# Kernel optimization log

Hardware: AMD Instinct MI355X
Metric: run time of the kernel (lower is better)

## Reference

```python
import jax, jax.numpy as jnp
import numpy as np

HID = 64
L = 5
N_NODES = 50000
N_EDGES = 1600000
N_GRAPHS = 4
EPS = 1e-5


def _ln(h, g, b):
    m = jnp.mean(h, axis=-1, keepdims=True)
    v = jnp.mean((h - m) ** 2, axis=-1, keepdims=True)
    return (h - m) * jax.lax.rsqrt(v + EPS) * g + b


def _lin_init(key, fan_in, fan_out):
    return jax.random.normal(key, (fan_in, fan_out), jnp.float32) / np.sqrt(fan_in)


def setup_inputs() -> dict:
    key = jax.random.key(0)
    ks = jax.random.split(key, 24)
    inp = {}
    inp['x'] = jax.random.normal(ks[0], (N_NODES, 8), jnp.float32)
    inp['edge_index'] = jax.random.randint(ks[1], (2, N_EDGES), 0, N_NODES)
    inp['edge_attr'] = jax.random.normal(ks[2], (N_EDGES, 5), jnp.float32)
    inp['batch'] = jnp.sort(jax.random.randint(ks[3], (N_NODES,), 0, N_GRAPHS))
    inp['case_params'] = jax.random.normal(ks[4], (N_GRAPHS, 4), jnp.float32)
    inp['bc_params'] = jax.random.normal(ks[5], (N_GRAPHS, 4), jnp.float32)
    # encoder
    inp['enc_W1'] = _lin_init(ks[6], 16, HID); inp['enc_b1'] = jnp.zeros((HID,))
    inp['enc_W2'] = _lin_init(ks[7], HID, HID); inp['enc_b2'] = jnp.zeros((HID,))
    inp['enc_g'] = jnp.ones((HID,)); inp['enc_be'] = jnp.zeros((HID,))
    # processor (stacked over L layers)
    ek = jax.random.split(ks[8], L); nk = jax.random.split(ks[9], L)
    ek2 = jax.random.split(ks[10], L); nk2 = jax.random.split(ks[11], L)
    inp['eW1'] = jnp.stack([_lin_init(ek[i], 2 * HID + 5, HID) for i in range(L)])
    inp['eb1'] = jnp.zeros((L, HID))
    inp['eW2'] = jnp.stack([_lin_init(ek2[i], HID, HID) for i in range(L)])
    inp['eb2'] = jnp.zeros((L, HID))
    inp['eg'] = jnp.ones((L, HID)); inp['ebe'] = jnp.zeros((L, HID))
    inp['nW1'] = jnp.stack([_lin_init(nk[i], 2 * HID, HID) for i in range(L)])
    inp['nb1'] = jnp.zeros((L, HID))
    inp['nW2'] = jnp.stack([_lin_init(nk2[i], HID, HID) for i in range(L)])
    inp['nb2'] = jnp.zeros((L, HID))
    inp['ng'] = jnp.ones((L, HID)); inp['nbe'] = jnp.zeros((L, HID))
    # decoders
    inp['dlW1'] = _lin_init(ks[12], HID, HID); inp['dlb1'] = jnp.zeros((HID,))
    inp['dlW2'] = _lin_init(ks[13], HID, 6); inp['dlb2'] = jnp.zeros((6,))
    inp['dgW1'] = _lin_init(ks[14], HID, HID // 2); inp['dgb1'] = jnp.zeros((HID // 2,))
    inp['dgW2'] = _lin_init(ks[15], HID // 2, 4); inp['dgb2'] = jnp.zeros((4,))
    return inp


def reference(x, edge_index, edge_attr, batch, case_params, bc_params,
              enc_W1, enc_b1, enc_W2, enc_b2, enc_g, enc_be,
              eW1, eb1, eW2, eb2, eg, ebe,
              nW1, nb1, nW2, nb2, ng, nbe,
              dlW1, dlb1, dlW2, dlb2, dgW1, dgb1, dgW2, dgb2):
    n_nodes = x.shape[0]
    n_graphs = case_params.shape[0]
    silu = jax.nn.silu
    # input concat: node feats + per-graph globals gathered by batch index
    gv = jnp.concatenate([case_params, bc_params], axis=1)  # [B, 8]
    h = jnp.concatenate([x, gv[batch]], axis=1)             # [N, 16]
    # encoder
    h = _ln(silu(h @ enc_W1 + enc_b1) @ enc_W2 + enc_b2, enc_g, enc_be)
    src, dst = edge_index[0], edge_index[1]  # PyG: x_j = src, x_i = dst
    n_layers = eW1.shape[0]
    for l in range(n_layers):
        xi = h[dst]  # [E, H] target
        xj = h[src]  # [E, H] source
        m = jnp.concatenate([xi, xj, edge_attr], axis=1)  # [E, 2H+5]
        m = _ln(silu(m @ eW1[l] + eb1[l]) @ eW2[l] + eb2[l], eg[l], ebe[l])
        agg = jax.ops.segment_sum(m, dst, num_segments=n_nodes)  # scatter-add
        t = jnp.concatenate([h, agg], axis=1)  # [N, 2H]
        h = h + _ln(silu(t @ nW1[l] + nb1[l]) @ nW2[l] + nb2[l], ng[l], nbe[l])
    out_local = silu(h @ dlW1 + dlb1) @ dlW2 + dlb2  # [N, 6]
    cnt = jax.ops.segment_sum(jnp.ones((n_nodes,), h.dtype), batch, num_segments=n_graphs)
    pooled = jax.ops.segment_sum(h, batch, num_segments=n_graphs) / jnp.maximum(cnt, 1.0)[:, None]
    out_global = silu(pooled @ dgW1 + dgb1) @ dgW2 + dgb2  # [B, 4]
    return (out_local, out_global)
```

## Files before the change

### kernel.cpp

```cpp
#include <hip/hip_runtime.h>
#include <cmath>

constexpr int NN = 50000;
constexpr int NE = 1600000;
constexpr int H  = 64;
constexpr int NL = 5;
constexpr int NG = 4;
constexpr int EIN = 2 * H + 5;
constexpr int NIN = 2 * H;

typedef short bf16x8 __attribute__((ext_vector_type(8)));
typedef float f32x4  __attribute__((ext_vector_type(4)));

__device__ __forceinline__ float silu_f(float x) {
    return x / (1.0f + __expf(-x));
}

__device__ __forceinline__ unsigned int f2bf(float f) {
    unsigned int u = __float_as_uint(f);
    u += 0x7fffu + ((u >> 16) & 1u);
    return u >> 16;
}
__device__ __forceinline__ unsigned int pack_bf16x2(float x, float y) {
    unsigned int r;
    asm("v_cvt_pk_bf16_f32 %0, %1, %2" : "=v"(r) : "v"(x), "v"(y));
    return r;
}

template <int CTRL>
__device__ __forceinline__ int dpp_i(int old, int v) {
    return __builtin_amdgcn_update_dpp(old, v, CTRL, 0xF, 0xF, false);
}

__global__ __launch_bounds__(256) void degree_kernel(
    const int* __restrict__ ei, int* __restrict__ deg)
{
    int e = blockIdx.x * 256 + threadIdx.x;
    if (e < NE) atomicAdd(&deg[ei[NE + e]], 1);
}

__global__ __launch_bounds__(1024) void scan1_kernel(
    const int* __restrict__ deg, int* __restrict__ off, int* __restrict__ bsum)
{
    __shared__ int sh[1024];
    const int tid = threadIdx.x;
    int i = blockIdx.x * 1024 + tid;
    int v = (i < NN) ? deg[i] : 0;
    sh[tid] = v;
    __syncthreads();
    for (int d = 1; d < 1024; d <<= 1) {
        int t = (tid >= d) ? sh[tid - d] : 0;
        __syncthreads();
        sh[tid] += t;
        __syncthreads();
    }
    if (i < NN) off[i] = sh[tid] - v;
    if (tid == 1023) bsum[blockIdx.x] = sh[1023];
}

__global__ __launch_bounds__(64) void scan2_kernel(
    const int* __restrict__ bsum, int* __restrict__ bbase, int nb)
{
    int lane = threadIdx.x;
    int v = (lane < nb) ? bsum[lane] : 0;
    int orig = v;
    for (int d = 1; d < 64; d <<= 1) {
        int t = __shfl_up(v, d);
        if (lane >= d) v += t;
    }
    bbase[lane] = v - orig;
}

__global__ __launch_bounds__(1024) void scan3_kernel(
    int* __restrict__ off, const int* __restrict__ bbase,
    int* __restrict__ cursor)
{
    int i = blockIdx.x * 1024 + threadIdx.x;
    if (i < NN) {
        int o = off[i] + bbase[blockIdx.x];
        off[i] = o;
        cursor[i] = o;
        if (i == NN - 1) off[NN] = NE;
    }
}

__global__ __launch_bounds__(256) void scatter_kernel(
    const int* __restrict__ ei, int* __restrict__ cursor,
    int* __restrict__ sidx, int* __restrict__ sdst, int* __restrict__ ssrc)
{
    int e = blockIdx.x * 256 + threadIdx.x;
    if (e < NE) {
        int d = ei[NE + e];
        int p = atomicAdd(&cursor[d], 1);
        sidx[p] = e;
        sdst[p] = d;
        ssrc[p] = ei[e];
    }
}

__global__ __launch_bounds__(256) void ea_pack_kernel(
    const float* __restrict__ ea, const int* __restrict__ sidx,
    uint4* __restrict__ ea_pk)
{
    int p = blockIdx.x * 256 + threadIdx.x;
    if (p < NE) {
        const float* s = ea + (size_t)sidx[p] * 5;
        uint4 v;
        v.x = pack_bf16x2(s[0], s[1]);
        v.y = pack_bf16x2(s[2], s[3]);
        v.z = pack_bf16x2(s[4], 0.0f);
        v.w = 0u;
        ea_pk[p] = v;
    }
}

__global__ __launch_bounds__(256) void pack_weights_kernel(
    const float* __restrict__ eW1, const float* __restrict__ eW2,
    const float* __restrict__ nW1, const float* __restrict__ nW2,
    const float* __restrict__ dlW1, const float* __restrict__ dlW2,
    short* __restrict__ eW1pk, short* __restrict__ eW2pk,
    short* __restrict__ nW1pk, short* __restrict__ nW2pk,
    short* __restrict__ dlW1pk, short* __restrict__ dlW2pk)
{
    int l = blockIdx.y;
    int t = blockIdx.x * 256 + threadIdx.x;
    if (t < 10240) {
        int j = t & 7, lane = (t >> 3) & 63, mt = (t >> 9) & 3, ks = t >> 11;
        int k  = ks * 32 + (lane >> 4) * 8 + j;
        int ch = mt * 16 + (lane & 15);
        float v = (k < EIN) ? eW1[(size_t)l * EIN * H + k * H + ch] : 0.0f;
        eW1pk[(size_t)l * 10240 + t] = (short)f2bf(v);
    } else if (t < 14336) {
        int t2 = t - 10240;
        int j = t2 & 7, lane = (t2 >> 3) & 63, mt = (t2 >> 9) & 3, ks = t2 >> 11;
        int k = ks * 32 + (lane >> 4) * 8 + j;
        int ch = mt * 16 + (lane & 15);
        eW2pk[(size_t)l * 4096 + t2] = (short)f2bf(eW2[(size_t)l * H * H + k * H + ch]);
    } else if (t < 22528) {
        int t3 = t - 14336;
        int j = t3 & 7, lane = (t3 >> 3) & 63, mt = (t3 >> 9) & 3, ks = t3 >> 11;
        int k = ks * 32 + (lane >> 4) * 8 + j;
        int ch = mt * 16 + (lane & 15);
        nW1pk[(size_t)l * 8192 + t3] = (short)f2bf(nW1[(size_t)l * NIN * H + k * H + ch]);
    } else if (t < 26624) {
        int t4 = t - 22528;
        int j = t4 & 7, lane = (t4 >> 3) & 63, mt = (t4 >> 9) & 3, ks = t4 >> 11;
        int k = ks * 32 + (lane >> 4) * 8 + j;
        int ch = mt * 16 + (lane & 15);
        nW2pk[(size_t)l * 4096 + t4] = (short)f2bf(nW2[(size_t)l * H * H + k * H + ch]);
    } else if (t < 30720) {
        if (l == 0) {
            int t5 = t - 26624;
            int j = t5 & 7, lane = (t5 >> 3) & 63, mt = (t5 >> 9) & 3, ks = t5 >> 11;
            int k = ks * 32 + (lane >> 4) * 8 + j;
            int ch = mt * 16 + (lane & 15);
            dlW1pk[t5] = (short)f2bf(dlW1[k * H + ch]);
        }
    } else if (t < 31744) {
        if (l == 0) {
            int t6 = t - 30720;
            int j = t6 & 7, lane = (t6 >> 3) & 63, ks = t6 >> 9;
            int k = ks * 32 + (lane >> 4) * 8 + j;
            int m = lane & 15;
            float v = (m < 6) ? dlW2[k * 6 + m] : 0.0f;
            dlW2pk[t6] = (short)f2bf(v);
        }
    }
}

__global__ __launch_bounds__(256) void encoder_kernel(
    const float* __restrict__ x, const int* __restrict__ batch,
    const float* __restrict__ case_p, const float* __restrict__ bc_p,
    const float* __restrict__ W1, const float* __restrict__ b1,
    const float* __restrict__ W2, const float* __restrict__ b2,
    const float* __restrict__ g, const float* __restrict__ be,
    float* __restrict__ h, unsigned int* __restrict__ h2)
{
    __shared__ float in_sh[64 * 17];
    __shared__ float m1_sh[64 * 65];
    __shared__ float red_sh[2 * 4 * 64];
    const int lane = threadIdx.x & 63;
    const int w    = threadIdx.x >> 6;
    const int wb   = __builtin_amdgcn_readfirstlane(w * 16);
    const int n0   = blockIdx.x * 64;

    for (int i = 0; i < 16; ++i) {
        int slot = w * 16 + i;
        int n = n0 + slot;
        if (n < NN && lane < 16) {
            float v;
            if (lane < 8) v = x[n * 8 + lane];
            else {
                int b = batch[n];
                v = (lane < 12) ? case_p[b * 4 + (lane - 8)]
                                : bc_p[b * 4 + (lane - 12)];
            }
            in_sh[slot * 17 + lane] = v;
        }
    }
    __syncthreads();

    float acc[16];
#pragma unroll
    for (int c = 0; c < 16; ++c) acc[c] = b1[wb + c];
    for (int k = 0; k < 16; ++k) {
        float a = in_sh[lane * 17 + k];
        const float4* wr = (const float4*)(W1 + k * 64 + wb);
        float4 w0 = wr[0], w1 = wr[1], w2 = wr[2], w3 = wr[3];
        acc[0]  = fmaf(a, w0.x, acc[0]);  acc[1]  = fmaf(a, w0.y, acc[1]);
        acc[2]  = fmaf(a, w0.z, acc[2]);  acc[3]  = fmaf(a, w0.w, acc[3]);
        acc[4]  = fmaf(a, w1.x, acc[4]);  acc[5]  = fmaf(a, w1.y, acc[5]);
        acc[6]  = fmaf(a, w1.z, acc[6]);  acc[7]  = fmaf(a, w1.w, acc[7]);
        acc[8]  = fmaf(a, w2.x, acc[8]);  acc[9]  = fmaf(a, w2.y, acc[9]);
        acc[10] = fmaf(a, w2.z, acc[10]); acc[11] = fmaf(a, w2.w, acc[11]);
        acc[12] = fmaf(a, w3.x, acc[12]); acc[13] = fmaf(a, w3.y, acc[13]);
        acc[14] = fmaf(a, w3.z, acc[14]); acc[15] = fmaf(a, w3.w, acc[15]);
    }
#pragma unroll
    for (int c = 0; c < 16; ++c) m1_sh[lane * 65 + wb + c] = silu_f(acc[c]);
    __syncthreads();

    float acc2[16];
#pragma unroll
    for (int c = 0; c < 16; ++c) acc2[c] = b2[wb + c];
    for (int k = 0; k < 64; ++k) {
        float a = m1_sh[lane * 65 + k];
        const float4* wr = (const float4*)(W2 + k * 64 + wb);
        float4 w0 = wr[0], w1 = wr[1], w2 = wr[2], w3 = wr[3];
        acc2[0]  = fmaf(a, w0.x, acc2[0]);  acc2[1]  = fmaf(a, w0.y, acc2[1]);
        acc2[2]  = fmaf(a, w0.z, acc2[2]);  acc2[3]  = fmaf(a, w0.w, acc2[3]);
        acc2[4]  = fmaf(a, w1.x, acc2[4]);  acc2[5]  = fmaf(a, w1.y, acc2[5]);
        acc2[6]  = fmaf(a, w1.z, acc2[6]);  acc2[7]  = fmaf(a, w1.w, acc2[7]);
        acc2[8]  = fmaf(a, w2.x, acc2[8]);  acc2[9]  = fmaf(a, w2.y, acc2[9]);
        acc2[10] = fmaf(a, w2.z, acc2[10]); acc2[11] = fmaf(a, w2.w, acc2[11]);
        acc2[12] = fmaf(a, w3.x, acc2[12]); acc2[13] = fmaf(a, w3.y, acc2[13]);
        acc2[14] = fmaf(a, w3.z, acc2[14]); acc2[15] = fmaf(a, w3.w, acc2[15]);
    }

    float s1 = 0.f, s2 = 0.f;
#pragma unroll
    for (int c = 0; c < 16; ++c) { s1 += acc2[c]; s2 += acc2[c] * acc2[c]; }
    red_sh[w * 64 + lane] = s1;
    red_sh[256 + w * 64 + lane] = s2;
    __syncthreads();
    float t1 = 0.f, t2 = 0.f;
#pragma unroll
    for (int j = 0; j < 4; ++j) {
        t1 += red_sh[j * 64 + lane];
        t2 += red_sh[256 + j * 64 + lane];
    }
    float mean = t1 * (1.0f / 64.0f);
    float var  = t2 * (1.0f / 64.0f) - mean * mean;
    float rstd = rsqrtf(var + 1e-5f);

    int n = n0 + lane;
    if (n < NN) {
        float vals[16];
#pragma unroll
        for (int c = 0; c < 16; ++c) {
            int ch = wb + c;
            vals[c] = (acc2[c] - mean) * rstd * g[ch] + be[ch];
            h[n * 64 + ch] = vals[c];
        }
        uint4 p0, p1;
        p0.x = pack_bf16x2(vals[0], vals[1]);   p0.y = pack_bf16x2(vals[2], vals[3]);
        p0.z = pack_bf16x2(vals[4], vals[5]);   p0.w = pack_bf16x2(vals[6], vals[7]);
        p1.x = pack_bf16x2(vals[8], vals[9]);   p1.y = pack_bf16x2(vals[10], vals[11]);
        p1.z = pack_bf16x2(vals[12], vals[13]); p1.w = pack_bf16x2(vals[14], vals[15]);
        *(uint4*)(h2 + (size_t)n * 32 + w * 8)     = p0;
        *(uint4*)(h2 + (size_t)n * 32 + w * 8 + 4) = p1;
    }
}

__global__ __launch_bounds__(256, 7) void edge_kernel(
    const unsigned int* __restrict__ h2,
    const int* __restrict__ sdst, const int* __restrict__ ssrc,
    const uint4* __restrict__ ea_pk,
    const short* __restrict__ W1pk, const float* __restrict__ b1,
    const short* __restrict__ W2pk, const float* __restrict__ b2,
    const float* __restrict__ g, const float* __restrict__ be,
    float* __restrict__ agg)
{
    __shared__ unsigned int lds[4 * 576];
    const int lane = threadIdx.x & 63;
    const int w    = threadIdx.x >> 6;
    const int quad = lane >> 4;
    const int l15  = lane & 15;
    const int tile = (blockIdx.x & 7) * 3125 + (blockIdx.x >> 3);
    const int e0   = tile * 64 + w * 16;
    unsigned int* MID = lds + w * 576;

    const int d_l = sdst[e0 + l15];
    const int s_l = ssrc[e0 + l15];

    union { uint4 u; bf16x8 b; } eacv;
    eacv.u = ea_pk[e0 + l15];
    const bf16x8 zfrag = {0, 0, 0, 0, 0, 0, 0, 0};
    const bf16x8 ks4frag = (quad == 0) ? eacv.b : zfrag;

    const unsigned int* drow = h2 + (size_t)d_l * 32 + quad * 4;
    const unsigned int* srow = h2 + (size_t)s_l * 32 + quad * 4;
    union { uint4 u; bf16x8 b; } bfA, bfB, bfC, bfD;
    bfA.u = *(const uint4*)(drow);
    bfB.u = *(const uint4*)(drow + 16);
    bfC.u = *(const uint4*)(srow);
    bfD.u = *(const uint4*)(srow + 16);

    f32x4 acc1[4] = {{0,0,0,0},{0,0,0,0},{0,0,0,0},{0,0,0,0}};
#define G1_STEP(KS, BFRAG)                                                    \
    {                                                                         \
        const short* apk = W1pk + (size_t)((KS) * 4) * 512 + lane * 8;        \
        _Pragma("unroll")                                                     \
        for (int mt = 0; mt < 4; ++mt) {                                      \
            bf16x8 afrag = *(const bf16x8*)(apk + mt * 512);                  \
            acc1[mt] = __builtin_amdgcn_mfma_f32_16x16x32_bf16(               \
                afrag, BFRAG, acc1[mt], 0, 0, 0);                             \
        }                                                                     \
    }
    G1_STEP(0, bfA.b)
    G1_STEP(1, bfB.b)
    G1_STEP(2, bfC.b)
    G1_STEP(3, bfD.b)
    G1_STEP(4, ks4frag)
#undef G1_STEP

#pragma unroll
    for (int mt = 0; mt < 4; ++mt) {
        int ch0 = mt * 16 + quad * 4;
        float v0 = silu_f(acc1[mt][0] + b1[ch0 + 0]);
        float v1 = silu_f(acc1[mt][1] + b1[ch0 + 1]);
        float v2 = silu_f(acc1[mt][2] + b1[ch0 + 2]);
        float v3 = silu_f(acc1[mt][3] + b1[ch0 + 3]);
        uint2 pk;
        pk.x = pack_bf16x2(v0, v1);
        pk.y = pack_bf16x2(v2, v3);
        *(uint2*)(MID + l15 * 36 + mt * 8 + quad * 2) = pk;
    }

    f32x4 acc2[4] = {{0,0,0,0},{0,0,0,0},{0,0,0,0},{0,0,0,0}};
    const unsigned int* mrow = MID + l15 * 36;
    for (int ks = 0; ks < 2; ++ks) {
        bf16x8 bfrag = *(const bf16x8*)(mrow + ks * 16 + quad * 4);
        const short* apk = W2pk + (size_t)(ks * 4) * 512 + lane * 8;
#pragma unroll
        for (int mt = 0; mt < 4; ++mt) {
            bf16x8 afrag = *(const bf16x8*)(apk + mt * 512);
            acc2[mt] = __builtin_amdgcn_mfma_f32_16x16x32_bf16(
                afrag, bfrag, acc2[mt], 0, 0, 0);
        }
    }

    float vals[16];
    float s1 = 0.f, s2 = 0.f;
#pragma unroll
    for (int mt = 0; mt < 4; ++mt) {
#pragma unroll
        for (int r = 0; r < 4; ++r) {
            int ch = mt * 16 + quad * 4 + r;
            float vv = acc2[mt][r] + b2[ch];
            vals[mt * 4 + r] = vv;
            s1 += vv; s2 += vv * vv;
        }
    }
    s1 += __shfl_xor(s1, 16); s1 += __shfl_xor(s1, 32);
    s2 += __shfl_xor(s2, 16); s2 += __shfl_xor(s2, 32);
    float mean = s1 * (1.0f / 64.0f);
    float var  = s2 * (1.0f / 64.0f) - mean * mean;
    float rstd = rsqrtf(var + 1e-5f);
#pragma unroll
    for (int mt = 0; mt < 4; ++mt) {
#pragma unroll
        for (int r = 0; r < 4; ++r) {
            int ch = mt * 16 + quad * 4 + r;
            vals[mt * 4 + r] = (vals[mt * 4 + r] - mean) * rstd * g[ch] + be[ch];
        }
    }

#define SEG_STEP(CTRL)                                                        \
    {                                                                         \
        int d_up = dpp_i<CTRL>(-1, d_l);                                      \
        float msk = (d_up == d_l) ? 1.0f : 0.0f;                              \
        _Pragma("unroll")                                                     \
        for (int c = 0; c < 16; ++c) {                                        \
            float vu = __int_as_float(dpp_i<CTRL>(0, __float_as_int(vals[c])));\
            vals[c] = fmaf(vu, msk, vals[c]);                                 \
        }                                                                     \
    }
    SEG_STEP(0x111)
    SEG_STEP(0x112)
    SEG_STEP(0x114)
    SEG_STEP(0x118)
#undef SEG_STEP
    int d_next = dpp_i<0x101>(-1, d_l);
    bool last = (d_next != d_l);
    if (last) {
#pragma unroll
        for (int mt = 0; mt < 4; ++mt) {
#pragma unroll
            for (int r = 0; r < 4; ++r) {
                int ch = mt * 16 + quad * 4 + r;
                atomicAdd(&agg[(size_t)d_l * 64 + ch], vals[mt * 4 + r]);
            }
        }
    }
}

__global__ __launch_bounds__(256, 6) void node_kernel(
    float* __restrict__ h, unsigned int* __restrict__ h2,
    const float* __restrict__ agg,
    const short* __restrict__ W1pk, const float* __restrict__ b1,
    const short* __restrict__ W2pk, const float* __restrict__ b2,
    const float* __restrict__ g, const float* __restrict__ be)
{
    __shared__ unsigned int lds[4 * 576];
    const int lane = threadIdx.x & 63;
    const int w    = threadIdx.x >> 6;
    const int quad = lane >> 4;
    const int l15  = lane & 15;
    const int n0   = blockIdx.x * 64 + w * 16;
    unsigned int* MID = lds + w * 576;

    int n_l = n0 + l15; if (n_l >= NN) n_l = NN - 1;

    const unsigned int* nrow = h2 + (size_t)n_l * 32 + quad * 4;
    union { uint4 u; bf16x8 b; } bfA, bfB;
    bfA.u = *(const uint4*)(nrow);
    bfB.u = *(const uint4*)(nrow + 16);
    const float* ap = agg + (size_t)n_l * 64 + quad * 8;
    float4 a0 = *(const float4*)(ap);
    float4 a1 = *(const float4*)(ap + 4);
    float4 a2 = *(const float4*)(ap + 32);
    float4 a3 = *(const float4*)(ap + 36);
    union { unsigned int u[4]; bf16x8 b; } bfC, bfD;
    bfC.u[0] = pack_bf16x2(a0.x, a0.y); bfC.u[1] = pack_bf16x2(a0.z, a0.w);
    bfC.u[2] = pack_bf16x2(a1.x, a1.y); bfC.u[3] = pack_bf16x2(a1.z, a1.w);
    bfD.u[0] = pack_bf16x2(a2.x, a2.y); bfD.u[1] = pack_bf16x2(a2.z, a2.w);
    bfD.u[2] = pack_bf16x2(a3.x, a3.y); bfD.u[3] = pack_bf16x2(a3.z, a3.w);

    f32x4 acc1[4] = {{0,0,0,0},{0,0,0,0},{0,0,0,0},{0,0,0,0}};
#define G1_STEP(KS, BFRAG)                                                    \
    {                                                                         \
        const short* apk = W1pk + (size_t)((KS) * 4) * 512 + lane * 8;        \
        _Pragma("unroll")                                                     \
        for (int mt = 0; mt < 4; ++mt) {                                      \
            bf16x8 afrag = *(const bf16x8*)(apk + mt * 512);                  \
            acc1[mt] = __builtin_amdgcn_mfma_f32_16x16x32_bf16(               \
                afrag, BFRAG, acc1[mt], 0, 0, 0);                             \
        }                                                                     \
    }
    G1_STEP(0, bfA.b)
    G1_STEP(1, bfB.b)
    G1_STEP(2, bfC.b)
    G1_STEP(3, bfD.b)
#undef G1_STEP

#pragma unroll
    for (int mt = 0; mt < 4; ++mt) {
        int ch0 = mt * 16 + quad * 4;
        float v0 = silu_f(acc1[mt][0] + b1[ch0 + 0]);
        float v1 = silu_f(acc1[mt][1] + b1[ch0 + 1]);
        float v2 = silu_f(acc1[mt][2] + b1[ch0 + 2]);
        float v3 = silu_f(acc1[mt][3] + b1[ch0 + 3]);
        uint2 pk;
        pk.x = pack_bf16x2(v0, v1);
        pk.y = pack_bf16x2(v2, v3);
        *(uint2*)(MID + l15 * 36 + mt * 8 + quad * 2) = pk;
    }

    f32x4 acc2[4] = {{0,0,0,0},{0,0,0,0},{0,0,0,0},{0,0,0,0}};
    const unsigned int* mrow = MID + l15 * 36;
    for (int ks = 0; ks < 2; ++ks) {
        bf16x8 bfrag = *(const bf16x8*)(mrow + ks * 16 + quad * 4);
        const short* apk = W2pk + (size_t)(ks * 4) * 512 + lane * 8;
#pragma unroll
        for (int mt = 0; mt < 4; ++mt) {
            bf16x8 afrag = *(const bf16x8*)(apk + mt * 512);
            acc2[mt] = __builtin_amdgcn_mfma_f32_16x16x32_bf16(
                afrag, bfrag, acc2[mt], 0, 0, 0);
        }
    }

    float vals[16];
    float s1 = 0.f, s2 = 0.f;
#pragma unroll
    for (int mt = 0; mt < 4; ++mt) {
#pragma unroll
        for (int r = 0; r < 4; ++r) {
            int ch = mt * 16 + quad * 4 + r;
            float vv = acc2[mt][r] + b2[ch];
            vals[mt * 4 + r] = vv;
            s1 += vv; s2 += vv * vv;
        }
    }
    s1 += __shfl_xor(s1, 16); s1 += __shfl_xor(s1, 32);
    s2 += __shfl_xor(s2, 16); s2 += __shfl_xor(s2, 32);
    float mean = s1 * (1.0f / 64.0f);
    float var  = s2 * (1.0f / 64.0f) - mean * mean;
    float rstd = rsqrtf(var + 1e-5f);

    int n = n0 + l15;
    if (n < NN) {
#pragma unroll
        for (int mt = 0; mt < 4; ++mt) {
            int ch0 = mt * 16 + quad * 4;
            float4 hv = *(const float4*)(h + (size_t)n * 64 + ch0);
            float o0 = hv.x + (vals[mt*4+0] - mean) * rstd * g[ch0+0] + be[ch0+0];
            float o1 = hv.y + (vals[mt*4+1] - mean) * rstd * g[ch0+1] + be[ch0+1];
            float o2 = hv.z + (vals[mt*4+2] - mean) * rstd * g[ch0+2] + be[ch0+2];
            float o3 = hv.w + (vals[mt*4+3] - mean) * rstd * g[ch0+3] + be[ch0+3];
            float4 st = {o0, o1, o2, o3};
            *(float4*)(h + (size_t)n * 64 + ch0) = st;
            uint2 pk;
            pk.x = pack_bf16x2(o0, o1);
            pk.y = pack_bf16x2(o2, o3);
            *(uint2*)(h2 + (size_t)n * 32 + mt * 8 + quad * 2) = pk;
        }
    }
}

__global__ __launch_bounds__(256, 7) void dec_local_kernel(
    const unsigned int* __restrict__ h2,
    const short* __restrict__ W1pk, const float* __restrict__ b1,
    const short* __restrict__ W2pk, const float* __restrict__ b2,
    float* __restrict__ out)
{
    __shared__ unsigned int lds[4 * 576];
    const int lane = threadIdx.x & 63;
    const int w    = threadIdx.x >> 6;
    const int quad = lane >> 4;
    const int l15  = lane & 15;
    const int n0   = blockIdx.x * 64 + w * 16;
    unsigned int* MID = lds + w * 576;

    int n_l = n0 + l15; if (n_l >= NN) n_l = NN - 1;
    const unsigned int* nrow = h2 + (size_t)n_l * 32 + quad * 4;
    union { uint4 u; bf16x8 b; } bfA, bfB;
    bfA.u = *(const uint4*)(nrow);
    bfB.u = *(const uint4*)(nrow + 16);

    f32x4 acc1[4] = {{0,0,0,0},{0,0,0,0},{0,0,0,0},{0,0,0,0}};
#define G1_STEP(KS, BFRAG)                                                    \
    {                                                                         \
        const short* apk = W1pk + (size_t)((KS) * 4) * 512 + lane * 8;        \
        _Pragma("unroll")                                                     \
        for (int mt = 0; mt < 4; ++mt) {                                      \
            bf16x8 afrag = *(const bf16x8*)(apk + mt * 512);                  \
            acc1[mt] = __builtin_amdgcn_mfma_f32_16x16x32_bf16(               \
                afrag, BFRAG, acc1[mt], 0, 0, 0);                             \
        }                                                                     \
    }
    G1_STEP(0, bfA.b)
    G1_STEP(1, bfB.b)
#undef G1_STEP

#pragma unroll
    for (int mt = 0; mt < 4; ++mt) {
        int ch0 = mt * 16 + quad * 4;
        float v0 = silu_f(acc1[mt][0] + b1[ch0 + 0]);
        float v1 = silu_f(acc1[mt][1] + b1[ch0 + 1]);
        float v2 = silu_f(acc1[mt][2] + b1[ch0 + 2]);
        float v3 = silu_f(acc1[mt][3] + b1[ch0 + 3]);
        uint2 pk;
        pk.x = pack_bf16x2(v0, v1);
        pk.y = pack_bf16x2(v2, v3);
        *(uint2*)(MID + l15 * 36 + mt * 8 + quad * 2) = pk;
    }

    f32x4 acc2 = {0, 0, 0, 0};
    const unsigned int* mrow = MID + l15 * 36;
    for (int ks = 0; ks < 2; ++ks) {
        bf16x8 bfrag = *(const bf16x8*)(mrow + ks * 16 + quad * 4);
        bf16x8 afrag = *(const bf16x8*)(W2pk + (size_t)ks * 512 + lane * 8);
        acc2 = __builtin_amdgcn_mfma_f32_16x16x32_bf16(afrag, bfrag, acc2, 0, 0, 0);
    }

    int n = n0 + l15;
    if (n < NN && quad < 2) {
#pragma unroll
        for (int r = 0; r < 4; ++r) {
            int ch = quad * 4 + r;
            if (ch < 6) out[(size_t)n * 6 + ch] = acc2[r] + b2[ch];
        }
    }
}

__global__ __launch_bounds__(256) void pool_kernel(
    const float* __restrict__ h, const int* __restrict__ batch,
    float* __restrict__ pooled, float* __restrict__ cnt)
{
    const int c   = threadIdx.x & 63;
    const int rep = blockIdx.x * 4 + (threadIdx.x >> 6);
    float acc[NG] = {0.f, 0.f, 0.f, 0.f};
    float cl[NG]  = {0.f, 0.f, 0.f, 0.f};
    for (int n = rep; n < NN; n += 1024) {
        int b = batch[n];
        float v = h[n * 64 + c];
#pragma unroll
        for (int gph = 0; gph < NG; ++gph) {
            if (b == gph) { acc[gph] += v; cl[gph] += 1.0f; }
        }
    }
#pragma unroll
    for (int gph = 0; gph < NG; ++gph) {
        atomicAdd(&pooled[gph * 64 + c], acc[gph]);
        if (c == 0) atomicAdd(&cnt[gph], cl[gph]);
    }
}

__global__ __launch_bounds__(256) void dec_global_kernel(
    const float* __restrict__ pooled, const float* __restrict__ cnt,
    const float* __restrict__ W1, const float* __restrict__ b1,
    const float* __restrict__ W2, const float* __restrict__ b2,
    float* __restrict__ out)
{
    __shared__ float mid_sh[4][32];
    const int lane = threadIdx.x & 63;
    const int gph  = threadIdx.x >> 6;
    float inv = 1.0f / fmaxf(cnt[gph], 1.0f);
    if (lane < 32) {
        float a = b1[lane];
        for (int k = 0; k < 64; ++k)
            a = fmaf(pooled[gph * 64 + k] * inv, W1[k * 32 + lane], a);
        mid_sh[gph][lane] = silu_f(a);
    }
    __syncthreads();
    if (lane < 4) {
        float o = b2[lane];
        for (int k = 0; k < 32; ++k)
            o = fmaf(mid_sh[gph][k], W2[k * 4 + lane], o);
        out[gph * 4 + lane] = o;
    }
}

extern "C" void kernel_launch(void* const* d_in, const int* in_sizes, int n_in,
                              void* d_out, int out_size, void* d_ws, size_t ws_size,
                              hipStream_t stream)
{
    const float* x      = (const float*)d_in[0];
    const int*   ei     = (const int*)  d_in[1];
    const float* ea     = (const float*)d_in[2];
    const int*   batch  = (const int*)  d_in[3];
    const float* case_p = (const float*)d_in[4];
    const float* bc_p   = (const float*)d_in[5];
    const float* enc_W1 = (const float*)d_in[6];
    const float* enc_b1 = (const float*)d_in[7];
    const float* enc_W2 = (const float*)d_in[8];
    const float* enc_b2 = (const float*)d_in[9];
    const float* enc_g  = (const float*)d_in[10];
    const float* enc_be = (const float*)d_in[11];
    const float* eW1    = (const float*)d_in[12];
    const float* eb1    = (const float*)d_in[13];
    const float* eW2    = (const float*)d_in[14];
    const float* eb2    = (const float*)d_in[15];
    const float* eg     = (const float*)d_in[16];
    const float* ebe    = (const float*)d_in[17];
    const float* nW1    = (const float*)d_in[18];
    const float* nb1    = (const float*)d_in[19];
    const float* nW2    = (const float*)d_in[20];
    const float* nb2    = (const float*)d_in[21];
    const float* ng     = (const float*)d_in[22];
    const float* nbe    = (const float*)d_in[23];
    const float* dlW1   = (const float*)d_in[24];
    const float* dlb1   = (const float*)d_in[25];
    const float* dlW2   = (const float*)d_in[26];
    const float* dlb2   = (const float*)d_in[27];
    const float* dgW1   = (const float*)d_in[28];
    const float* dgb1   = (const float*)d_in[29];
    const float* dgW2   = (const float*)d_in[30];
    const float* dgb2   = (const float*)d_in[31];

    float* out = (float*)d_out;

    char* ws = (char*)d_ws;
    size_t off_b = 0;
    auto alloc = [&](size_t bytes) {
        void* p = ws + off_b;
        off_b = (off_b + bytes + 255) & ~(size_t)255;
        return p;
    };
    const size_t hBytes = (size_t)NN * H * sizeof(float);
    float*        h      = (float*)alloc(hBytes);
    float*        agg    = (float*)alloc(hBytes);
    unsigned int* h2     = (unsigned int*)alloc((size_t)NN * 32 * 4);
    float*        pooled = (float*)alloc(256 * sizeof(float));
    float*        cnt    = (float*)alloc(4 * sizeof(float));
    int*          deg    = (int*)alloc((NN + 1) * sizeof(int));
    int*          offs   = (int*)alloc((NN + 1) * sizeof(int));
    int*          cursor = (int*)alloc((NN + 1) * sizeof(int));
    int*          bsum   = (int*)alloc(64 * sizeof(int));
    int*          bbase  = (int*)alloc(64 * sizeof(int));
    int*          sidx   = (int*)alloc((size_t)NE * sizeof(int));
    int*          sdst   = (int*)alloc((size_t)NE * sizeof(int));
    int*          ssrc   = (int*)alloc((size_t)NE * sizeof(int));
    uint4*        ea_pk  = (uint4*)alloc((size_t)NE * sizeof(uint4));
    short*        eW1pk  = (short*)alloc((size_t)NL * 10240 * sizeof(short));
    short*        eW2pk  = (short*)alloc((size_t)NL * 4096 * sizeof(short));
    short*        nW1pk  = (short*)alloc((size_t)NL * 8192 * sizeof(short));
    short*        nW2pk  = (short*)alloc((size_t)NL * 4096 * sizeof(short));
    short*        dlW1pk = (short*)alloc(4096 * sizeof(short));
    short*        dlW2pk = (short*)alloc(1024 * sizeof(short));

    hipMemsetAsync(pooled, 0, (256 + 4 + 64) * sizeof(float), stream);
    hipMemsetAsync(deg, 0, (NN + 1) * sizeof(int), stream);

    const int NB = (NN + 1023) / 1024;
    degree_kernel<<<(NE + 255) / 256, 256, 0, stream>>>(ei, deg);
    scan1_kernel<<<NB, 1024, 0, stream>>>(deg, offs, bsum);
    scan2_kernel<<<1, 64, 0, stream>>>(bsum, bbase, NB);
    scan3_kernel<<<NB, 1024, 0, stream>>>(offs, bbase, cursor);
    scatter_kernel<<<(NE + 255) / 256, 256, 0, stream>>>(ei, cursor, sidx, sdst, ssrc);
    ea_pack_kernel<<<(NE + 255) / 256, 256, 0, stream>>>(ea, sidx, ea_pk);
    pack_weights_kernel<<<dim3(124, NL), 256, 0, stream>>>(
        eW1, eW2, nW1, nW2, dlW1, dlW2,
        eW1pk, eW2pk, nW1pk, nW2pk, dlW1pk, dlW2pk);

    const int nodeBlocks = (NN + 63) / 64;
    encoder_kernel<<<nodeBlocks, 256, 0, stream>>>(
        x, batch, case_p, bc_p, enc_W1, enc_b1, enc_W2, enc_b2, enc_g, enc_be,
        h, h2);

    for (int l = 0; l < NL; ++l) {
        hipMemsetAsync(agg, 0, hBytes, stream);
        edge_kernel<<<NE / 64, 256, 0, stream>>>(
            h2, sdst, ssrc, ea_pk,
            eW1pk + (size_t)l * 10240, eb1 + l * H,
            eW2pk + (size_t)l * 4096,  eb2 + l * H,
            eg + l * H, ebe + l * H, agg);
        node_kernel<<<nodeBlocks, 256, 0, stream>>>(
            h, h2, agg,
            nW1pk + (size_t)l * 8192, nb1 + l * H,
            nW2pk + (size_t)l * 4096, nb2 + l * H,
            ng + l * H, nbe + l * H);
    }

    dec_local_kernel<<<nodeBlocks, 256, 0, stream>>>(
        h2, dlW1pk, dlb1, dlW2pk, dlb2, out);
    pool_kernel<<<256, 256, 0, stream>>>(h, batch, pooled, cnt);
    dec_global_kernel<<<1, 256, 0, stream>>>(pooled, cnt, dgW1, dgb1, dgW2, dgb2,
                                             out + (size_t)NN * 6);
}
```

Measured before the change: 1.590 ms.

## Make edge kernel node-centric over CSR, hoist destination GEMM term, drop atomics

```diff
diff --git a/kernel.cpp b/kernel.cpp
--- a/kernel.cpp
+++ b/kernel.cpp
@@ -86,14 +86,13 @@
 
 __global__ __launch_bounds__(256) void scatter_kernel(
     const int* __restrict__ ei, int* __restrict__ cursor,
-    int* __restrict__ sidx, int* __restrict__ sdst, int* __restrict__ ssrc)
+    int* __restrict__ sidx, int* __restrict__ ssrc)
 {
     int e = blockIdx.x * 256 + threadIdx.x;
     if (e < NE) {
         int d = ei[NE + e];
         int p = atomicAdd(&cursor[d], 1);
         sidx[p] = e;
-        sdst[p] = d;
         ssrc[p] = ei[e];
     }
 }
@@ -272,142 +271,191 @@
     }
 }
 
-__global__ __launch_bounds__(256, 7) void edge_kernel(
+__global__ __launch_bounds__(256, 4) void edge_kernel(
     const unsigned int* __restrict__ h2,
-    const int* __restrict__ sdst, const int* __restrict__ ssrc,
+    const int* __restrict__ offs, const int* __restrict__ ssrc,
     const uint4* __restrict__ ea_pk,
     const short* __restrict__ W1pk, const float* __restrict__ b1,
     const short* __restrict__ W2pk, const float* __restrict__ b2,
     const float* __restrict__ g, const float* __restrict__ be,
-    float* __restrict__ agg)
+    unsigned int* __restrict__ agg2)
 {
     __shared__ unsigned int lds[4 * 576];
     const int lane = threadIdx.x & 63;
     const int w    = threadIdx.x >> 6;
     const int quad = lane >> 4;
     const int l15  = lane & 15;
-    const int tile = (blockIdx.x & 7) * 3125 + (blockIdx.x >> 3);
-    const int e0   = tile * 64 + w * 16;
+    const int node = blockIdx.x * 4 + w;
     unsigned int* MID = lds + w * 576;
 
-    const int d_l = sdst[e0 + l15];
-    const int s_l = ssrc[e0 + l15];
-
-    union { uint4 u; bf16x8 b; } eacv;
-    eacv.u = ea_pk[e0 + l15];
-    const bf16x8 zfrag = {0, 0, 0, 0, 0, 0, 0, 0};
-    const bf16x8 ks4frag = (quad == 0) ? eacv.b : zfrag;
-
-    const unsigned int* drow = h2 + (size_t)d_l * 32 + quad * 4;
-    const unsigned int* srow = h2 + (size_t)s_l * 32 + quad * 4;
-    union { uint4 u; bf16x8 b; } bfA, bfB, bfC, bfD;
+    const int start = offs[node];
+    const int end   = offs[node + 1];
+
+    const unsigned int* drow = h2 + (size_t)node * 32 + quad * 4;
+    union { uint4 u; bf16x8 b; } bfA, bfB;
     bfA.u = *(const uint4*)(drow);
     bfB.u = *(const uint4*)(drow + 16);
-    bfC.u = *(const uint4*)(srow);
-    bfD.u = *(const uint4*)(srow + 16);
-
-    f32x4 acc1[4] = {{0,0,0,0},{0,0,0,0},{0,0,0,0},{0,0,0,0}};
-#define G1_STEP(KS, BFRAG)                                                    \
-    {                                                                         \
-        const short* apk = W1pk + (size_t)((KS) * 4) * 512 + lane * 8;        \
-        _Pragma("unroll")                                                     \
-        for (int mt = 0; mt < 4; ++mt) {                                      \
-            bf16x8 afrag = *(const bf16x8*)(apk + mt * 512);                  \
-            acc1[mt] = __builtin_amdgcn_mfma_f32_16x16x32_bf16(               \
-                afrag, BFRAG, acc1[mt], 0, 0, 0);                             \
-        }                                                                     \
-    }
-    G1_STEP(0, bfA.b)
-    G1_STEP(1, bfB.b)
-    G1_STEP(2, bfC.b)
-    G1_STEP(3, bfD.b)
-    G1_STEP(4, ks4frag)
-#undef G1_STEP
-
-#pragma unroll
-    for (int mt = 0; mt < 4; ++mt) {
-        int ch0 = mt * 16 + quad * 4;
-        float v0 = silu_f(acc1[mt][0] + b1[ch0 + 0]);
-        float v1 = silu_f(acc1[mt][1] + b1[ch0 + 1]);
-        float v2 = silu_f(acc1[mt][2] + b1[ch0 + 2]);
-        float v3 = silu_f(acc1[mt][3] + b1[ch0 + 3]);
-        uint2 pk;
-        pk.x = pack_bf16x2(v0, v1);
-        pk.y = pack_bf16x2(v2, v3);
-        *(uint2*)(MID + l15 * 36 + mt * 8 + quad * 2) = pk;
-    }
-
-    f32x4 acc2[4] = {{0,0,0,0},{0,0,0,0},{0,0,0,0},{0,0,0,0}};
-    const unsigned int* mrow = MID + l15 * 36;
-    for (int ks = 0; ks < 2; ++ks) {
-        bf16x8 bfrag = *(const bf16x8*)(mrow + ks * 16 + quad * 4);
-        const short* apk = W2pk + (size_t)(ks * 4) * 512 + lane * 8;
-#pragma unroll
-        for (int mt = 0; mt < 4; ++mt) {
-            bf16x8 afrag = *(const bf16x8*)(apk + mt * 512);
-            acc2[mt] = __builtin_amdgcn_mfma_f32_16x16x32_bf16(
-                afrag, bfrag, acc2[mt], 0, 0, 0);
-        }
-    }
-
-    float vals[16];
-    float s1 = 0.f, s2 = 0.f;
-#pragma unroll
-    for (int mt = 0; mt < 4; ++mt) {
-#pragma unroll
-        for (int r = 0; r < 4; ++r) {
-            int ch = mt * 16 + quad * 4 + r;
-            float vv = acc2[mt][r] + b2[ch];
-            vals[mt * 4 + r] = vv;
-            s1 += vv; s2 += vv * vv;
-        }
-    }
-    s1 += __shfl_xor(s1, 16); s1 += __shfl_xor(s1, 32);
-    s2 += __shfl_xor(s2, 16); s2 += __shfl_xor(s2, 32);
-    float mean = s1 * (1.0f / 64.0f);
-    float var  = s2 * (1.0f / 64.0f) - mean * mean;
-    float rstd = rsqrtf(var + 1e-5f);
-#pragma unroll
-    for (int mt = 0; mt < 4; ++mt) {
-#pragma unroll
-        for (int r = 0; r < 4; ++r) {
-            int ch = mt * 16 + quad * 4 + r;
-            vals[mt * 4 + r] = (vals[mt * 4 + r] - mean) * rstd * g[ch] + be[ch];
-        }
-    }
-
-#define SEG_STEP(CTRL)                                                        \
-    {                                                                         \
-        int d_up = dpp_i<CTRL>(-1, d_l);                                      \
-        float msk = (d_up == d_l) ? 1.0f : 0.0f;                              \
-        _Pragma("unroll")                                                     \
-        for (int c = 0; c < 16; ++c) {                                        \
-            float vu = __int_as_float(dpp_i<CTRL>(0, __float_as_int(vals[c])));\
-            vals[c] = fmaf(vu, msk, vals[c]);                                 \
-        }                                                                     \
-    }
-    SEG_STEP(0x111)
-    SEG_STEP(0x112)
-    SEG_STEP(0x114)
-    SEG_STEP(0x118)
-#undef SEG_STEP
-    int d_next = dpp_i<0x101>(-1, d_l);
-    bool last = (d_next != d_l);
-    if (last) {
+
+    f32x4 acc1d[4] = {{0,0,0,0},{0,0,0,0},{0,0,0,0},{0,0,0,0}};
+    {
+        const short* apk0 = W1pk + lane * 8;
+        const short* apk1 = W1pk + (size_t)(1 * 4) * 512 + lane * 8;
+#pragma unroll
+        for (int mt = 0; mt < 4; ++mt) {
+            bf16x8 afrag = *(const bf16x8*)(apk0 + mt * 512);
+            acc1d[mt] = __builtin_amdgcn_mfma_f32_16x16x32_bf16(
+                afrag, bfA.b, acc1d[mt], 0, 0, 0);
+        }
+#pragma unroll
+        for (int mt = 0; mt < 4; ++mt) {
+            bf16x8 afrag = *(const bf16x8*)(apk1 + mt * 512);
+            acc1d[mt] = __builtin_amdgcn_mfma_f32_16x16x32_bf16(
+                afrag, bfB.b, acc1d[mt], 0, 0, 0);
+        }
+#pragma unroll
+        for (int mt = 0; mt < 4; ++mt) {
+            int ch0 = mt * 16 + quad * 4;
+#pragma unroll
+            for (int r = 0; r < 4; ++r) acc1d[mt][r] += b1[ch0 + r];
+        }
+    }
+
+    const bf16x8 zfrag = {0, 0, 0, 0, 0, 0, 0, 0};
+    float accN[16];
+#pragma unroll
+    for (int c = 0; c < 16; ++c) accN[c] = 0.f;
+
+    for (int e0 = start; e0 < end; e0 += 16) {
+        int e = e0 + l15;
+        bool valid = (e < end);
+        int ec = valid ? e : (end - 1);
+        int s_l = ssrc[ec];
+        const unsigned int* srow = h2 + (size_t)s_l * 32 + quad * 4;
+        union { uint4 u; bf16x8 b; } bfC, bfD, eacv;
+        bfC.u = *(const uint4*)(srow);
+        bfD.u = *(const uint4*)(srow + 16);
+        eacv.u = ea_pk[ec];
+        bf16x8 ks4frag = (quad == 0) ? eacv.b : zfrag;
+
+        f32x4 acc1[4];
+        {
+            const short* apk = W1pk + (size_t)(2 * 4) * 512 + lane * 8;
+#pragma unroll
+            for (int mt = 0; mt < 4; ++mt) {
+                bf16x8 afrag = *(const bf16x8*)(apk + mt * 512);
+                acc1[mt] = __builtin_amdgcn_mfma_f32_16x16x32_bf16(
+                    afrag, bfC.b, acc1d[mt], 0, 0, 0);
+            }
+        }
+        {
+            const short* apk = W1pk + (size_t)(3 * 4) * 512 + lane * 8;
+#pragma unroll
+            for (int mt = 0; mt < 4; ++mt) {
+                bf16x8 afrag = *(const bf16x8*)(apk + mt * 512);
+                acc1[mt] = __builtin_amdgcn_mfma_f32_16x16x32_bf16(
+                    afrag, bfD.b, acc1[mt], 0, 0, 0);
+            }
+        }
+        {
+            const short* apk = W1pk + (size_t)(4 * 4) * 512 + lane * 8;
+#pragma unroll
+            for (int mt = 0; mt < 4; ++mt) {
+                bf16x8 afrag = *(const bf16x8*)(apk + mt * 512);
+                acc1[mt] = __builtin_amdgcn_mfma_f32_16x16x32_bf16(
+                    afrag, ks4frag, acc1[mt], 0, 0, 0);
+            }
+        }
+
+#pragma unroll
+        for (int mt = 0; mt < 4; ++mt) {
+            float v0 = silu_f(acc1[mt][0]);
+            float v1 = silu_f(acc1[mt][1]);
+            float v2 = silu_f(acc1[mt][2]);
+            float v3 = silu_f(acc1[mt][3]);
+            uint2 pk;
+            pk.x = pack_bf16x2(v0, v1);
+            pk.y = pack_bf16x2(v2, v3);
+            *(uint2*)(MID + l15 * 36 + mt * 8 + quad * 2) = pk;
+        }
+
+        f32x4 acc2[4];
+#pragma unroll
+        for (int mt = 0; mt < 4; ++mt) {
+            int ch0 = mt * 16 + quad * 4;
+            f32x4 c0 = {b2[ch0 + 0], b2[ch0 + 1], b2[ch0 + 2], b2[ch0 + 3]};
+            acc2[mt] = c0;
+        }
+        const unsigned int* mrow = MID + l15 * 36;
+        for (int ks = 0; ks < 2; ++ks) {
+            bf16x8 bfrag = *(const bf16x8*)(mrow + ks * 16 + quad * 4);
+            const short* apk = W2pk + (size_t)(ks * 4) * 512 + lane * 8;
+#pragma unroll
+            for (int mt = 0; mt < 4; ++mt) {
+                bf16x8 afrag = *(const bf16x8*)(apk + mt * 512);
+                acc2[mt] = __builtin_amdgcn_mfma_f32_16x16x32_bf16(
+                    afrag, bfrag, acc2[mt], 0, 0, 0);
+            }
+        }
+
+        float vals[16];
+        float s1 = 0.f, s2 = 0.f;
+#pragma unroll
+        for (int mt = 0; mt < 4; ++mt) {
+#pragma unroll
+            for (int r = 0; r < 4; ++r) {
+                float vv = acc2[mt][r];
+                vals[mt * 4 + r] = vv;
+                s1 += vv; s2 += vv * vv;
+            }
+        }
+        s1 += __shfl_xor(s1, 16); s1 += __shfl_xor(s1, 32);
+        s2 += __shfl_xor(s2, 16); s2 += __shfl_xor(s2, 32);
+        float mean = s1 * (1.0f / 64.0f);
+        float var  = s2 * (1.0f / 64.0f) - mean * mean;
+        float rstd = rsqrtf(var + 1e-5f);
+        float mr   = -mean * rstd;
+        float maskf = valid ? 1.0f : 0.0f;
 #pragma unroll
         for (int mt = 0; mt < 4; ++mt) {
 #pragma unroll
             for (int r = 0; r < 4; ++r) {
                 int ch = mt * 16 + quad * 4 + r;
-                atomicAdd(&agg[(size_t)d_l * 64 + ch], vals[mt * 4 + r]);
+                float t = fmaf(vals[mt * 4 + r], rstd, mr);
+                vals[mt * 4 + r] = fmaf(t, g[ch], be[ch]) * maskf;
             }
+        }
+
+#define RED_STEP(CTRL)                                                        \
+        {                                                                     \
+            _Pragma("unroll")                                                 \
+            for (int c = 0; c < 16; ++c)                                      \
+                vals[c] += __int_as_float(                                    \
+                    dpp_i<CTRL>(0, __float_as_int(vals[c])));                 \
+        }
+        RED_STEP(0x111)
+        RED_STEP(0x112)
+        RED_STEP(0x114)
+        RED_STEP(0x118)
+#undef RED_STEP
+#pragma unroll
+        for (int c = 0; c < 16; ++c) accN[c] += vals[c];
+    }
+
+    if (l15 == 15) {
+        unsigned int* arow = agg2 + (size_t)node * 32 + quad * 2;
+#pragma unroll
+        for (int mt = 0; mt < 4; ++mt) {
+            uint2 pk;
+            pk.x = pack_bf16x2(accN[mt * 4 + 0], accN[mt * 4 + 1]);
+            pk.y = pack_bf16x2(accN[mt * 4 + 2], accN[mt * 4 + 3]);
+            *(uint2*)(arow + mt * 8) = pk;
         }
     }
 }
 
 __global__ __launch_bounds__(256, 6) void node_kernel(
     float* __restrict__ h, unsigned int* __restrict__ h2,
-    const float* __restrict__ agg,
+    const unsigned int* __restrict__ agg2,
     const short* __restrict__ W1pk, const float* __restrict__ b1,
     const short* __restrict__ W2pk, const float* __restrict__ b2,
     const float* __restrict__ g, const float* __restrict__ be)
@@ -423,19 +471,12 @@
     int n_l = n0 + l15; if (n_l >= NN) n_l = NN - 1;
 
     const unsigned int* nrow = h2 + (size_t)n_l * 32 + quad * 4;
-    union { uint4 u; bf16x8 b; } bfA, bfB;
+    union { uint4 u; bf16x8 b; } bfA, bfB, bfC, bfD;
     bfA.u = *(const uint4*)(nrow);
     bfB.u = *(const uint4*)(nrow + 16);
-    const float* ap = agg + (size_t)n_l * 64 + quad * 8;
-    float4 a0 = *(const float4*)(ap);
-    float4 a1 = *(const float4*)(ap + 4);
-    float4 a2 = *(const float4*)(ap + 32);
-    float4 a3 = *(const float4*)(ap + 36);
-    union { unsigned int u[4]; bf16x8 b; } bfC, bfD;
-    bfC.u[0] = pack_bf16x2(a0.x, a0.y); bfC.u[1] = pack_bf16x2(a0.z, a0.w);
-    bfC.u[2] = pack_bf16x2(a1.x, a1.y); bfC.u[3] = pack_bf16x2(a1.z, a1.w);
-    bfD.u[0] = pack_bf16x2(a2.x, a2.y); bfD.u[1] = pack_bf16x2(a2.z, a2.w);
-    bfD.u[2] = pack_bf16x2(a3.x, a3.y); bfD.u[3] = pack_bf16x2(a3.z, a3.w);
+    const unsigned int* arow = agg2 + (size_t)n_l * 32 + quad * 4;
+    bfC.u = *(const uint4*)(arow);
+    bfD.u = *(const uint4*)(arow + 16);
 
     f32x4 acc1[4] = {{0,0,0,0},{0,0,0,0},{0,0,0,0},{0,0,0,0}};
 #define G1_STEP(KS, BFRAG)                                                    \
@@ -680,8 +721,8 @@
     };
     const size_t hBytes = (size_t)NN * H * sizeof(float);
     float*        h      = (float*)alloc(hBytes);
-    float*        agg    = (float*)alloc(hBytes);
     unsigned int* h2     = (unsigned int*)alloc((size_t)NN * 32 * 4);
+    unsigned int* agg2   = (unsigned int*)alloc((size_t)NN * 32 * 4);
     float*        pooled = (float*)alloc(256 * sizeof(float));
     float*        cnt    = (float*)alloc(4 * sizeof(float));
     int*          deg    = (int*)alloc((NN + 1) * sizeof(int));
@@ -690,7 +731,6 @@
     int*          bsum   = (int*)alloc(64 * sizeof(int));
     int*          bbase  = (int*)alloc(64 * sizeof(int));
     int*          sidx   = (int*)alloc((size_t)NE * sizeof(int));
-    int*          sdst   = (int*)alloc((size_t)NE * sizeof(int));
     int*          ssrc   = (int*)alloc((size_t)NE * sizeof(int));
     uint4*        ea_pk  = (uint4*)alloc((size_t)NE * sizeof(uint4));
     short*        eW1pk  = (short*)alloc((size_t)NL * 10240 * sizeof(short));
@@ -708,7 +748,7 @@
     scan1_kernel<<<NB, 1024, 0, stream>>>(deg, offs, bsum);
     scan2_kernel<<<1, 64, 0, stream>>>(bsum, bbase, NB);
     scan3_kernel<<<NB, 1024, 0, stream>>>(offs, bbase, cursor);
-    scatter_kernel<<<(NE + 255) / 256, 256, 0, stream>>>(ei, cursor, sidx, sdst, ssrc);
+    scatter_kernel<<<(NE + 255) / 256, 256, 0, stream>>>(ei, cursor, sidx, ssrc);
     ea_pack_kernel<<<(NE + 255) / 256, 256, 0, stream>>>(ea, sidx, ea_pk);
     pack_weights_kernel<<<dim3(124, NL), 256, 0, stream>>>(
         eW1, eW2, nW1, nW2, dlW1, dlW2,
@@ -719,15 +759,15 @@
         x, batch, case_p, bc_p, enc_W1, enc_b1, enc_W2, enc_b2, enc_g, enc_be,
         h, h2);
 
+    const int edgeBlocks = NN / 4;
     for (int l = 0; l < NL; ++l) {
-        hipMemsetAsync(agg, 0, hBytes, stream);
-        edge_kernel<<<NE / 64, 256, 0, stream>>>(
-            h2, sdst, ssrc, ea_pk,
+        edge_kernel<<<edgeBlocks, 256, 0, stream>>>(
+            h2, offs, ssrc, ea_pk,
             eW1pk + (size_t)l * 10240, eb1 + l * H,
             eW2pk + (size_t)l * 4096,  eb2 + l * H,
-            eg + l * H, ebe + l * H, agg);
+            eg + l * H, ebe + l * H, agg2);
         node_kernel<<<nodeBlocks, 256, 0, stream>>>(
-            h, h2, agg,
+            h, h2, agg2,
             nW1pk + (size_t)l * 8192, nb1 + l * H,
             nW2pk + (size_t)l * 4096, nb2 + l * H,
             ng + l * H, nbe + l * H);
```

Result: slower. 1.867 ms (+17.4%).

## Process five edge tiles per wave with software-prefetched gathers in edge kernel

Applied to the files above, without the earlier changes.

```diff
diff --git a/kernel.cpp b/kernel.cpp
--- a/kernel.cpp
+++ b/kernel.cpp
@@ -272,7 +272,7 @@
     }
 }
 
-__global__ __launch_bounds__(256, 7) void edge_kernel(
+__global__ __launch_bounds__(256, 4) void edge_kernel(
     const unsigned int* __restrict__ h2,
     const int* __restrict__ sdst, const int* __restrict__ ssrc,
     const uint4* __restrict__ ea_pk,
@@ -286,27 +286,30 @@
     const int w    = threadIdx.x >> 6;
     const int quad = lane >> 4;
     const int l15  = lane & 15;
-    const int tile = (blockIdx.x & 7) * 3125 + (blockIdx.x >> 3);
-    const int e0   = tile * 64 + w * 16;
+    const int tile = (blockIdx.x & 7) * 625 + (blockIdx.x >> 3);
+    const int base = tile * 320 + w * 80;
     unsigned int* MID = lds + w * 576;
-
-    const int d_l = sdst[e0 + l15];
-    const int s_l = ssrc[e0 + l15];
-
-    union { uint4 u; bf16x8 b; } eacv;
-    eacv.u = ea_pk[e0 + l15];
     const bf16x8 zfrag = {0, 0, 0, 0, 0, 0, 0, 0};
-    const bf16x8 ks4frag = (quad == 0) ? eacv.b : zfrag;
-
-    const unsigned int* drow = h2 + (size_t)d_l * 32 + quad * 4;
-    const unsigned int* srow = h2 + (size_t)s_l * 32 + quad * 4;
-    union { uint4 u; bf16x8 b; } bfA, bfB, bfC, bfD;
-    bfA.u = *(const uint4*)(drow);
-    bfB.u = *(const uint4*)(drow + 16);
-    bfC.u = *(const uint4*)(srow);
-    bfD.u = *(const uint4*)(srow + 16);
-
-    f32x4 acc1[4] = {{0,0,0,0},{0,0,0,0},{0,0,0,0},{0,0,0,0}};
+
+    int   pd[5], ps[5];
+    uint4 pea[5], rA[5], rB[5], rC[5], rD[5];
+
+#define IDX_LOAD(J)                                                           \
+    {                                                                         \
+        int ei = base + (J) * 16 + l15;                                       \
+        pd[J] = sdst[ei];                                                     \
+        ps[J] = ssrc[ei];                                                     \
+        pea[J] = ea_pk[ei];                                                   \
+    }
+#define ROW_LOAD(J)                                                           \
+    {                                                                         \
+        const unsigned int* dr = h2 + (size_t)pd[J] * 32 + quad * 4;          \
+        const unsigned int* sr = h2 + (size_t)ps[J] * 32 + quad * 4;          \
+        rA[J] = *(const uint4*)(dr);                                          \
+        rB[J] = *(const uint4*)(dr + 16);                                     \
+        rC[J] = *(const uint4*)(sr);                                          \
+        rD[J] = *(const uint4*)(sr + 16);                                     \
+    }
 #define G1_STEP(KS, BFRAG)                                                    \
     {                                                                         \
         const short* apk = W1pk + (size_t)((KS) * 4) * 512 + lane * 8;        \
@@ -317,92 +320,115 @@
                 afrag, BFRAG, acc1[mt], 0, 0, 0);                             \
         }                                                                     \
     }
-    G1_STEP(0, bfA.b)
-    G1_STEP(1, bfB.b)
-    G1_STEP(2, bfC.b)
-    G1_STEP(3, bfD.b)
-    G1_STEP(4, ks4frag)
-#undef G1_STEP
-
-#pragma unroll
-    for (int mt = 0; mt < 4; ++mt) {
-        int ch0 = mt * 16 + quad * 4;
-        float v0 = silu_f(acc1[mt][0] + b1[ch0 + 0]);
-        float v1 = silu_f(acc1[mt][1] + b1[ch0 + 1]);
-        float v2 = silu_f(acc1[mt][2] + b1[ch0 + 2]);
-        float v3 = silu_f(acc1[mt][3] + b1[ch0 + 3]);
-        uint2 pk;
-        pk.x = pack_bf16x2(v0, v1);
-        pk.y = pack_bf16x2(v2, v3);
-        *(uint2*)(MID + l15 * 36 + mt * 8 + quad * 2) = pk;
-    }
-
-    f32x4 acc2[4] = {{0,0,0,0},{0,0,0,0},{0,0,0,0},{0,0,0,0}};
-    const unsigned int* mrow = MID + l15 * 36;
-    for (int ks = 0; ks < 2; ++ks) {
-        bf16x8 bfrag = *(const bf16x8*)(mrow + ks * 16 + quad * 4);
-        const short* apk = W2pk + (size_t)(ks * 4) * 512 + lane * 8;
+
+    IDX_LOAD(0)
+    ROW_LOAD(0)
+    IDX_LOAD(1)
+
+#pragma unroll
+    for (int j = 0; j < 5; ++j) {
+        union { uint4 u; bf16x8 b; } uA, uB, uC, uD, uE;
+        uA.u = rA[j]; uB.u = rB[j]; uC.u = rC[j]; uD.u = rD[j];
+        uE.u = pea[j];
+        bf16x8 ks4frag = (quad == 0) ? uE.b : zfrag;
+
+        f32x4 acc1[4] = {{0,0,0,0},{0,0,0,0},{0,0,0,0},{0,0,0,0}};
+        G1_STEP(0, uA.b)
+        G1_STEP(1, uB.b)
+        G1_STEP(2, uC.b)
+        G1_STEP(3, uD.b)
+        G1_STEP(4, ks4frag)
+
+        if (j < 4) ROW_LOAD(j + 1)
+        if (j < 3) IDX_LOAD(j + 2)
+
 #pragma unroll
         for (int mt = 0; mt < 4; ++mt) {
-            bf16x8 afrag = *(const bf16x8*)(apk + mt * 512);
-            acc2[mt] = __builtin_amdgcn_mfma_f32_16x16x32_bf16(
-                afrag, bfrag, acc2[mt], 0, 0, 0);
-        }
-    }
-
-    float vals[16];
-    float s1 = 0.f, s2 = 0.f;
-#pragma unroll
-    for (int mt = 0; mt < 4; ++mt) {
-#pragma unroll
-        for (int r = 0; r < 4; ++r) {
-            int ch = mt * 16 + quad * 4 + r;
-            float vv = acc2[mt][r] + b2[ch];
-            vals[mt * 4 + r] = vv;
-            s1 += vv; s2 += vv * vv;
-        }
-    }
-    s1 += __shfl_xor(s1, 16); s1 += __shfl_xor(s1, 32);
-    s2 += __shfl_xor(s2, 16); s2 += __shfl_xor(s2, 32);
-    float mean = s1 * (1.0f / 64.0f);
-    float var  = s2 * (1.0f / 64.0f) - mean * mean;
-    float rstd = rsqrtf(var + 1e-5f);
-#pragma unroll
-    for (int mt = 0; mt < 4; ++mt) {
-#pragma unroll
-        for (int r = 0; r < 4; ++r) {
-            int ch = mt * 16 + quad * 4 + r;
-            vals[mt * 4 + r] = (vals[mt * 4 + r] - mean) * rstd * g[ch] + be[ch];
-        }
-    }
-
-#define SEG_STEP(CTRL)                                                        \
-    {                                                                         \
-        int d_up = dpp_i<CTRL>(-1, d_l);                                      \
-        float msk = (d_up == d_l) ? 1.0f : 0.0f;                              \
-        _Pragma("unroll")                                                     \
-        for (int c = 0; c < 16; ++c) {                                        \
-            float vu = __int_as_float(dpp_i<CTRL>(0, __float_as_int(vals[c])));\
-            vals[c] = fmaf(vu, msk, vals[c]);                                 \
-        }                                                                     \
-    }
-    SEG_STEP(0x111)
-    SEG_STEP(0x112)
-    SEG_STEP(0x114)
-    SEG_STEP(0x118)
-#undef SEG_STEP
-    int d_next = dpp_i<0x101>(-1, d_l);
-    bool last = (d_next != d_l);
-    if (last) {
+            int ch0 = mt * 16 + quad * 4;
+            float v0 = silu_f(acc1[mt][0] + b1[ch0 + 0]);
+            float v1 = silu_f(acc1[mt][1] + b1[ch0 + 1]);
+            float v2 = silu_f(acc1[mt][2] + b1[ch0 + 2]);
+            float v3 = silu_f(acc1[mt][3] + b1[ch0 + 3]);
+            uint2 pk;
+            pk.x = pack_bf16x2(v0, v1);
+            pk.y = pack_bf16x2(v2, v3);
+            *(uint2*)(MID + l15 * 36 + mt * 8 + quad * 2) = pk;
+        }
+
+        f32x4 acc2[4] = {{0,0,0,0},{0,0,0,0},{0,0,0,0},{0,0,0,0}};
+        const unsigned int* mrow = MID + l15 * 36;
+#pragma unroll
+        for (int ks = 0; ks < 2; ++ks) {
+            bf16x8 bfrag = *(const bf16x8*)(mrow + ks * 16 + quad * 4);
+            const short* apk = W2pk + (size_t)(ks * 4) * 512 + lane * 8;
+#pragma unroll
+            for (int mt = 0; mt < 4; ++mt) {
+                bf16x8 afrag = *(const bf16x8*)(apk + mt * 512);
+                acc2[mt] = __builtin_amdgcn_mfma_f32_16x16x32_bf16(
+                    afrag, bfrag, acc2[mt], 0, 0, 0);
+            }
+        }
+
+        float vals[16];
+        float s1 = 0.f, s2 = 0.f;
 #pragma unroll
         for (int mt = 0; mt < 4; ++mt) {
 #pragma unroll
             for (int r = 0; r < 4; ++r) {
                 int ch = mt * 16 + quad * 4 + r;
-                atomicAdd(&agg[(size_t)d_l * 64 + ch], vals[mt * 4 + r]);
+                float vv = acc2[mt][r] + b2[ch];
+                vals[mt * 4 + r] = vv;
+                s1 += vv; s2 += vv * vv;
             }
         }
-    }
+        s1 += __shfl_xor(s1, 16); s1 += __shfl_xor(s1, 32);
+        s2 += __shfl_xor(s2, 16); s2 += __shfl_xor(s2, 32);
+        float mean = s1 * (1.0f / 64.0f);
+        float var  = s2 * (1.0f / 64.0f) - mean * mean;
+        float rstd = rsqrtf(var + 1e-5f);
+#pragma unroll
+        for (int mt = 0; mt < 4; ++mt) {
+#pragma unroll
+            for (int r = 0; r < 4; ++r) {
+                int ch = mt * 16 + quad * 4 + r;
+                vals[mt * 4 + r] =
+                    (vals[mt * 4 + r] - mean) * rstd * g[ch] + be[ch];
+            }
+        }
+
+        int d_l = pd[j];
+#define SEG_STEP(CTRL)                                                        \
+        {                                                                     \
+            int d_up = dpp_i<CTRL>(-1, d_l);                                  \
+            float msk = (d_up == d_l) ? 1.0f : 0.0f;                          \
+            _Pragma("unroll")                                                 \
+            for (int c = 0; c < 16; ++c) {                                    \
+                float vu = __int_as_float(                                    \
+                    dpp_i<CTRL>(0, __float_as_int(vals[c])));                 \
+                vals[c] = fmaf(vu, msk, vals[c]);                             \
+            }                                                                 \
+        }
+        SEG_STEP(0x111)
+        SEG_STEP(0x112)
+        SEG_STEP(0x114)
+        SEG_STEP(0x118)
+#undef SEG_STEP
+        int d_next = dpp_i<0x101>(-1, d_l);
+        bool last = (d_next != d_l);
+        if (last) {
+#pragma unroll
+            for (int mt = 0; mt < 4; ++mt) {
+#pragma unroll
+                for (int r = 0; r < 4; ++r) {
+                    int ch = mt * 16 + quad * 4 + r;
+                    atomicAdd(&agg[(size_t)d_l * 64 + ch], vals[mt * 4 + r]);
+                }
+            }
+        }
+    }
+#undef IDX_LOAD
+#undef ROW_LOAD
+#undef G1_STEP
 }
 
 __global__ __launch_bounds__(256, 6) void node_kernel(
@@ -719,9 +745,10 @@
         x, batch, case_p, bc_p, enc_W1, enc_b1, enc_W2, enc_b2, enc_g, enc_be,
         h, h2);
 
+    const int edgeBlocks = NE / 320;
     for (int l = 0; l < NL; ++l) {
         hipMemsetAsync(agg, 0, hBytes, stream);
-        edge_kernel<<<NE / 64, 256, 0, stream>>>(
+        edge_kernel<<<edgeBlocks, 256, 0, stream>>>(
             h2, sdst, ssrc, ea_pk,
             eW1pk + (size_t)l * 10240, eb1 + l * H,
             eW2pk + (size_t)l * 4096,  eb2 + l * H,
```

After: 1.660 ms. 4.4% more time.
